# Kernel optimization log

Hardware: AMD Instinct MI355X
Metric: run time of the kernel (lower is better)

The kernel has to match this reference:

```python
import jax, jax.numpy as jnp
import numpy as np

POS_IDX = np.array([0, 2, 4, 10, 14, 20, 22, 24])   # +w taps on 5x5 ring
NEG_IDX = np.array([6, 7, 8, 11, 13, 16, 17, 18])   # -w taps on inner 3x3 ring (center stays 0)


def setup_inputs() -> dict:
    key = jax.random.key(0)
    kx, kw = jax.random.split(key)
    x = jax.random.normal(kx, (16, 256, 128, 128), dtype=jnp.float32)
    weight = jax.random.normal(kw, (256, 1, 3, 3), dtype=jnp.float32) * 0.1
    return {"x": x, "weight": weight}


def _build_rpdc_kernel(weight):
    # weight: [C, 1, 3, 3] -> sparse 5x5 kernel [C, 1, 5, 5]
    C = weight.shape[0]
    w = weight.reshape(C, 1, 9)
    tap = w[:, :, 1:]  # taps 1..8 (skip w[0]); center of 5x5 is forced to 0
    buf = jnp.zeros((C, 1, 25), dtype=weight.dtype)
    buf = buf.at[:, :, POS_IDX].set(tap)
    buf = buf.at[:, :, NEG_IDX].set(-tap)
    return buf.reshape(C, 1, 5, 5)


def reference(x, weight):
    # Depthwise conv (groups = in_channels), dilation=1 -> padding = 2 (same conv)
    C = weight.shape[0]
    kernel = _build_rpdc_kernel(weight)
    return jax.lax.conv_general_dilated(
        x, kernel,
        window_strides=(1, 1),
        padding=[(2, 2), (2, 2)],
        rhs_dilation=(1, 1),
        dimension_numbers=("NCHW", "OIHW", "NCHW"),
        feature_group_count=C,
    )
```

## Files before the change

### kernel.cpp

```cpp
#include <hip/hip_runtime.h>


#define HH 128
#define WW 128

__global__ __launch_bounds__(256, 8) void rpdc_kernel(
    const float* __restrict__ x, const float* __restrict__ wt,
    float* __restrict__ out, int C)
{
    const int tid = threadIdx.x;
    const int w = tid & (WW - 1);
    const int plane = blockIdx.x * 2 + (tid >> 7);
    const int c = plane & (C - 1);

    const float* wp = wt + (size_t)c * 9;
    const float t0 = wp[1], t1 = wp[2], t2 = wp[3], t3 = wp[4],
                t4 = wp[5], t5 = wp[6], t6 = wp[7], t7 = wp[8];

    const float* xp = x + (size_t)plane * (HH * WW);
    float* op = out + (size_t)plane * (HH * WW) + w;

    const int o0 = (w >= 2) ? (w - 2) : 0;
    const int o1 = (w >= 1) ? (w - 1) : 0;
    const int o2 = w;
    const int o3 = (w <= WW - 2) ? (w + 1) : (WW - 1);
    const int o4 = (w <= WW - 3) ? (w + 2) : (WW - 1);
    const float m0 = (w >= 2) ? 1.f : 0.f;
    const float m1 = (w >= 1) ? 1.f : 0.f;
    const float m3 = (w <= WW - 2) ? 1.f : 0.f;
    const float m4 = (w <= WW - 3) ? 1.f : 0.f;

    float a[5], b[5], cc[5], d[5], e[5];
#pragma unroll
    for (int k = 0; k < 5; ++k) { a[k] = 0.f; b[k] = 0.f; }

    {
        const float* p = xp;
        cc[0] = p[o0] * m0; cc[1] = p[o1] * m1; cc[2] = p[o2];
        cc[3] = p[o3] * m3; cc[4] = p[o4] * m4;
        p += WW;
        d[0] = p[o0] * m0; d[1] = p[o1] * m1; d[2] = p[o2];
        d[3] = p[o3] * m3; d[4] = p[o4] * m4;
        p += WW;
        e[0] = p[o0] * m0; e[1] = p[o1] * m1; e[2] = p[o2];
        e[3] = p[o3] * m3; e[4] = p[o4] * m4;
    }

    const float* pn = xp + 3 * WW;
#pragma unroll 4
    for (int h = 0; h < HH; ++h) {
        float r = t0 * (a[0] - b[1]);
        r += t1 * (a[2] - b[2]);
        r += t2 * (a[4] - b[3]);
        r += t3 * (cc[0] - cc[1]);
        r += t4 * (cc[4] - cc[3]);
        r += t5 * (e[0] - d[1]);
        r += t6 * (e[2] - d[2]);
        r += t7 * (e[4] - d[3]);
        op[h * WW] = r;

#pragma unroll
        for (int k = 0; k < 5; ++k) { a[k] = b[k]; b[k] = cc[k]; cc[k] = d[k]; d[k] = e[k]; }

        if (h + 3 < HH) {
            e[0] = pn[o0] * m0; e[1] = pn[o1] * m1; e[2] = pn[o2];
            e[3] = pn[o3] * m3; e[4] = pn[o4] * m4;
            pn += WW;
        } else {
#pragma unroll
            for (int k = 0; k < 5; ++k) e[k] = 0.f;
        }
    }
}

extern "C" void kernel_launch(void* const* d_in, const int* in_sizes, int n_in,
                              void* d_out, int out_size, void* d_ws, size_t ws_size,
                              hipStream_t stream) {
    const float* x = (const float*)d_in[0];
    const float* wt = (const float*)d_in[1];
    float* out = (float*)d_out;

    const int C = in_sizes[1] / 9;
    const int planes = in_sizes[0] / (HH * WW);

    dim3 grid(planes / 2);
    dim3 block(256);
    rpdc_kernel<<<grid, block, 0, stream>>>(x, wt, out, C);
}
```

Before: 464.0 us.

## Process four columns per thread with float4 loads and shuffle halos

Each thread now handles four adjacent columns, loading rows as float4 and fetching left/right halo values from neighbouring lanes via 32-wide shuffles instead of five scalar loads. Each plane is split into two 64-row halves, with 32-lane groups each handling one half, so the grid covers four planes per block. Loads and stores become vectorised, which cuts memory instructions, and the split adds parallelism per plane. In exchange the halo rows at the half boundary are loaded twice, shuffle overhead is added, and register use rises, so launch bounds drop to 6 blocks per unit.

Measured after the change: 781.6 us. 68.4% more time.

```diff
diff --git a/kernel.cpp b/kernel.cpp
--- a/kernel.cpp
+++ b/kernel.cpp
@@ -3,87 +3,87 @@
 
 #define HH 128
 #define WW 128
+#define CH 64
 
-__global__ __launch_bounds__(256, 8) void rpdc_kernel(
+__global__ __launch_bounds__(256, 6) void rpdc_kernel(
     const float* __restrict__ x, const float* __restrict__ wt,
     float* __restrict__ out, int C)
 {
-    const int tid = threadIdx.x;
-    const int w = tid & (WW - 1);
-    const int plane = blockIdx.x * 2 + (tid >> 7);
-    const int c = plane & (C - 1);
+    const int tid  = threadIdx.x;
+    const int lane = tid & 31;
+    const int unit = tid >> 5;
+    const int plane = blockIdx.x * 4 + (unit >> 1);
+    const int half  = unit & 1;
+    const int h0    = half * CH;
+    const int c     = plane & (C - 1);
 
     const float* wp = wt + (size_t)c * 9;
     const float t0 = wp[1], t1 = wp[2], t2 = wp[3], t3 = wp[4],
                 t4 = wp[5], t5 = wp[6], t6 = wp[7], t7 = wp[8];
 
-    const float* xp = x + (size_t)plane * (HH * WW);
-    float* op = out + (size_t)plane * (HH * WW) + w;
+    const float* xp = x   + (size_t)plane * (HH * WW) + lane * 4;
+    float*       op = out + (size_t)plane * (HH * WW) + (size_t)h0 * WW + lane * 4;
 
-    const int o0 = (w >= 2) ? (w - 2) : 0;
-    const int o1 = (w >= 1) ? (w - 1) : 0;
-    const int o2 = w;
-    const int o3 = (w <= WW - 2) ? (w + 1) : (WW - 1);
-    const int o4 = (w <= WW - 3) ? (w + 2) : (WW - 1);
-    const float m0 = (w >= 2) ? 1.f : 0.f;
-    const float m1 = (w >= 1) ? 1.f : 0.f;
-    const float m3 = (w <= WW - 2) ? 1.f : 0.f;
-    const float m4 = (w <= WW - 3) ? 1.f : 0.f;
+    const float eL = (lane == 0)  ? 0.f : 1.f;
+    const float eR = (lane == 31) ? 0.f : 1.f;
 
-    float a[5], b[5], cc[5], d[5], e[5];
+    float A[8], B[8], Cw[8], D[8], E[8];
+
+#define LOADROW(r, W8) do {                                             \
+    const int _rc = (r) < 0 ? 0 : ((r) > HH - 1 ? HH - 1 : (r));        \
+    const float _m = ((r) >= 0 && (r) < HH) ? 1.f : 0.f;                \
+    float4 _v = *(const float4*)(xp + (size_t)_rc * WW);                \
+    _v.x *= _m; _v.y *= _m; _v.z *= _m; _v.w *= _m;                     \
+    (W8)[2] = _v.x; (W8)[3] = _v.y; (W8)[4] = _v.z; (W8)[5] = _v.w;     \
+    (W8)[0] = __shfl(_v.z, lane - 1, 32) * eL;                          \
+    (W8)[1] = __shfl(_v.w, lane - 1, 32) * eL;                          \
+    (W8)[6] = __shfl(_v.x, lane + 1, 32) * eR;                          \
+    (W8)[7] = __shfl(_v.y, lane + 1, 32) * eR;                          \
+  } while (0)
+
+    LOADROW(h0 - 2, A);
+    LOADROW(h0 - 1, B);
+    LOADROW(h0,     Cw);
+    LOADROW(h0 + 1, D);
+    LOADROW(h0 + 2, E);
+
+#pragma unroll 4
+    for (int i = 0; i < CH; ++i) {
+        float res[4];
 #pragma unroll
-    for (int k = 0; k < 5; ++k) { a[k] = 0.f; b[k] = 0.f; }
-
-    {
-        const float* p = xp;
-        cc[0] = p[o0] * m0; cc[1] = p[o1] * m1; cc[2] = p[o2];
-        cc[3] = p[o3] * m3; cc[4] = p[o4] * m4;
-        p += WW;
-        d[0] = p[o0] * m0; d[1] = p[o1] * m1; d[2] = p[o2];
-        d[3] = p[o3] * m3; d[4] = p[o4] * m4;
-        p += WW;
-        e[0] = p[o0] * m0; e[1] = p[o1] * m1; e[2] = p[o2];
-        e[3] = p[o3] * m3; e[4] = p[o4] * m4;
-    }
-
-    const float* pn = xp + 3 * WW;
-#pragma unroll 4
-    for (int h = 0; h < HH; ++h) {
-        float r = t0 * (a[0] - b[1]);
-        r += t1 * (a[2] - b[2]);
-        r += t2 * (a[4] - b[3]);
-        r += t3 * (cc[0] - cc[1]);
-        r += t4 * (cc[4] - cc[3]);
-        r += t5 * (e[0] - d[1]);
-        r += t6 * (e[2] - d[2]);
-        r += t7 * (e[4] - d[3]);
-        op[h * WW] = r;
+        for (int j = 0; j < 4; ++j) {
+            float r = t0 * (A[j]     - B[j + 1]);
+            r += t1 * (A[j + 2] - B[j + 2]);
+            r += t2 * (A[j + 4] - B[j + 3]);
+            r += t3 * (Cw[j]    - Cw[j + 1]);
+            r += t4 * (Cw[j + 4] - Cw[j + 3]);
+            r += t5 * (E[j]     - D[j + 1]);
+            r += t6 * (E[j + 2] - D[j + 2]);
+            r += t7 * (E[j + 4] - D[j + 3]);
+            res[j] = r;
+        }
+        float4 o = { res[0], res[1], res[2], res[3] };
+        *(float4*)(op + (size_t)i * WW) = o;
 
 #pragma unroll
-        for (int k = 0; k < 5; ++k) { a[k] = b[k]; b[k] = cc[k]; cc[k] = d[k]; d[k] = e[k]; }
+        for (int k = 0; k < 8; ++k) { A[k] = B[k]; B[k] = Cw[k]; Cw[k] = D[k]; D[k] = E[k]; }
 
-        if (h + 3 < HH) {
-            e[0] = pn[o0] * m0; e[1] = pn[o1] * m1; e[2] = pn[o2];
-            e[3] = pn[o3] * m3; e[4] = pn[o4] * m4;
-            pn += WW;
-        } else {
-#pragma unroll
-            for (int k = 0; k < 5; ++k) e[k] = 0.f;
-        }
+        LOADROW(h0 + i + 3, E);
     }
+#undef LOADROW
 }
 
 extern "C" void kernel_launch(void* const* d_in, const int* in_sizes, int n_in,
                               void* d_out, int out_size, void* d_ws, size_t ws_size,
                               hipStream_t stream) {
-    const float* x = (const float*)d_in[0];
+    const float* x  = (const float*)d_in[0];
     const float* wt = (const float*)d_in[1];
     float* out = (float*)d_out;
 
     const int C = in_sizes[1] / 9;
     const int planes = in_sizes[0] / (HH * WW);
 
-    dim3 grid(planes / 2);
+    dim3 grid(planes / 4);
     dim3 block(256);
     rpdc_kernel<<<grid, block, 0, stream>>>(x, wt, out, C);
 }
```
